# Kernel tuning notes

Hardware: AMD Instinct MI355X
Metric: run time of the kernel (lower is better)

Reference implementation:

```python
import jax, jax.numpy as jnp
import numpy as np

VOCAB, EMBED, HIDDEN = 32000, 512, 1024
BATCH, SRC_LEN = 64, 1024

def _xavier(key, shape):
    fan_out, fan_in = shape
    bound = float(np.sqrt(6.0 / (fan_in + fan_out)))
    return jax.random.uniform(key, shape, jnp.float32, -bound, bound)

def setup_inputs() -> dict:
    key = jax.random.key(0)
    k0, k1, k2, k3, k4 = jax.random.split(key, 5)
    src = jax.random.randint(k0, (BATCH, SRC_LEN), 0, VOCAB)
    emb = jax.random.normal(k1, (VOCAB, EMBED), jnp.float32)  # nn.Embedding default N(0,1)
    Wx = _xavier(k2, (4 * HIDDEN, EMBED))                     # x2h weight (out,in)
    bx = jax.random.uniform(k3, (4 * HIDDEN,), jnp.float32,
                            -1.0 / np.sqrt(EMBED), 1.0 / np.sqrt(EMBED))  # Linear default bias init
    Wh = _xavier(k4, (4 * HIDDEN, HIDDEN))                    # h2h weight, no bias
    return {"src": src, "emb": emb, "Wx": Wx, "bx": bx, "Wh": Wh}

def reference(src, emb, Wx, bx, Wh):
    B, T = src.shape
    H = Wh.shape[1]
    embedded = emb[src]                      # (B, T, E)
    # Precompute input projections for all steps: (T, B, 4H)
    x_proj = jnp.einsum('bte,ge->tbg', embedded, Wx) + bx

    def step(carry, xg):
        h, c = carry
        gates = xg + h @ Wh.T                # (B, 4H)
        i, f, o, g = jnp.split(gates, 4, axis=1)
        i = jax.nn.sigmoid(i)
        f = jax.nn.sigmoid(f)
        o = jax.nn.sigmoid(o)
        g = jnp.tanh(g)
        c = f * c + i * g
        h = o * jnp.tanh(c)
        return (h, c), None

    init = (jnp.zeros((B, H), jnp.float32), jnp.zeros((B, H), jnp.float32))
    (h_t, c_t), _ = jax.lax.scan(step, init, x_proj)
    return (h_t, c_t)
```

## Files before the change

### kernel.cpp

```cpp
#include <hip/hip_runtime.h>

typedef unsigned short u16;
typedef unsigned int   u32;
typedef unsigned long long u64;
typedef __attribute__((ext_vector_type(8))) __bf16 bf16x8;
typedef __attribute__((ext_vector_type(4))) float   f32x4;

#define B_   64
#define H_   1024
#define E_   512
#define G4_  4096
#define T_   1024
#define NWG  64

__device__ __forceinline__ u16 f2b(float f){
  union { float f; u32 u; } v; v.f = f;
  u32 r = v.u + 0x7fffu + ((v.u >> 16) & 1u);
  return (u16)(r >> 16);
}
__device__ __forceinline__ float b2f(u16 u){
  union { u32 u; float f; } v; v.u = ((u32)u) << 16;
  return v.f;
}
__device__ __forceinline__ float sigf(float x){
  return 1.0f / (1.0f + __expf(-x));
}
__device__ __forceinline__ float tanhf_s(float x){
  float ax = fabsf(x);
  float e  = __expf(2.0f * ax);
  float t  = 1.0f - 2.0f / (e + 1.0f);
  return copysignf(t, x);
}
__device__ __forceinline__ void gload_lds16(const void* g, void* l){
  __builtin_amdgcn_global_load_lds(
      (const __attribute__((address_space(1))) u32*)g,
      (__attribute__((address_space(3))) u32*)l, 16, 0, 0);
}

__global__ __launch_bounds__(256) void cvt_bf16(const float* __restrict__ in,
                                                u16* __restrict__ out, int n){
  int i = (blockIdx.x * 256 + threadIdx.x) * 4;
  if (i >= n) return;
  float4 v = *reinterpret_cast<const float4*>(in + i);
  ushort4 o;
  o.x = f2b(v.x); o.y = f2b(v.y); o.z = f2b(v.z); o.w = f2b(v.w);
  *reinterpret_cast<ushort4*>(out + i) = o;
}

__global__ __launch_bounds__(256) void emb_gather(const int* __restrict__ src,
                                                  const float* __restrict__ emb,
                                                  u16* __restrict__ embSeg, int t0){
  int idx = blockIdx.x * 256 + threadIdx.x;
  int m  = idx >> 7;
  int e4 = (idx & 127) << 2;
  int b = m & 63, ts = m >> 6;
  int tok = src[b * T_ + t0 + ts];
  float4 v = *reinterpret_cast<const float4*>(emb + (size_t)tok * E_ + e4);
  ushort4 o;
  o.x = f2b(v.x); o.y = f2b(v.y); o.z = f2b(v.z); o.w = f2b(v.w);
  *reinterpret_cast<ushort4*>(embSeg + (size_t)m * E_ + e4) = o;
}

__global__ __launch_bounds__(256) void xproj_gemm(const u16* __restrict__ embSeg,
                                                  const u16* __restrict__ WxB,
                                                  const float* __restrict__ bx,
                                                  u16* __restrict__ xp){
  __shared__ alignas(16) u16 Al[2][128][64];
  __shared__ alignas(16) u16 Bl[2][128][64];
  const int tid  = threadIdx.x;
  const int lane = tid & 63, wv = tid >> 6;
  const int wm = wv >> 1, wn = wv & 1;
  const int m0 = blockIdx.y * 128, n0 = blockIdx.x * 128;

  const int srow_w = wv * 8 + (lane >> 3);
  const int csrc   = (lane & 7) ^ (lane >> 3);

  auto stage = [&](int buf, int kb){
    const int kbase = kb * 64 + csrc * 8;
    #pragma unroll
    for (int it = 0; it < 4; ++it){
      const u16* ga = embSeg + (size_t)(m0 + it * 32 + srow_w) * E_ + kbase;
      gload_lds16(ga, &Al[buf][it * 32 + wv * 8][0]);
    }
    #pragma unroll
    for (int it = 0; it < 4; ++it){
      const u16* gb = WxB + (size_t)(n0 + it * 32 + srow_w) * E_ + kbase;
      gload_lds16(gb, &Bl[buf][it * 32 + wv * 8][0]);
    }
  };

  f32x4 acc[4][4] = {};
  stage(0, 0);
  __syncthreads();
  for (int kb = 0; kb < 8; ++kb){
    const int cur = kb & 1;
    if (kb < 7) stage(cur ^ 1, kb + 1);
    #pragma unroll
    for (int kk = 0; kk < 2; ++kk){
      bf16x8 af[4], bfr[4];
      #pragma unroll
      for (int i = 0; i < 4; ++i){
        int row = wm * 64 + i * 16 + (lane & 15);
        int cp  = (kk * 4 + (lane >> 4)) ^ (row & 7);
        af[i] = *reinterpret_cast<const bf16x8*>(&Al[cur][row][cp * 8]);
      }
      #pragma unroll
      for (int j = 0; j < 4; ++j){
        int row = wn * 64 + j * 16 + (lane & 15);
        int cp  = (kk * 4 + (lane >> 4)) ^ (row & 7);
        bfr[j] = *reinterpret_cast<const bf16x8*>(&Bl[cur][row][cp * 8]);
      }
      #pragma unroll
      for (int i = 0; i < 4; ++i)
        #pragma unroll
        for (int j = 0; j < 4; ++j)
          acc[i][j] = __builtin_amdgcn_mfma_f32_16x16x32_bf16(af[i], bfr[j], acc[i][j], 0, 0, 0);
    }
    __syncthreads();
  }

  float bxv[4];
  #pragma unroll
  for (int j = 0; j < 4; ++j) bxv[j] = bx[n0 + wn * 64 + j * 16 + (lane & 15)];
  #pragma unroll
  for (int i = 0; i < 4; ++i){
    int mrow = m0 + wm * 64 + i * 16 + ((lane >> 4) << 2);
    #pragma unroll
    for (int r = 0; r < 4; ++r){
      size_t base = (size_t)(mrow + r) * G4_ + n0 + wn * 64 + (lane & 15);
      #pragma unroll
      for (int j = 0; j < 4; ++j)
        xp[base + j * 16] = f2b(acc[i][j][r] + bxv[j]);
    }
  }
}

__global__ __launch_bounds__(256, 1) void lstm_rec(const float* __restrict__ Wh,
                                                   const u16* __restrict__ xp,
                                                   u16* __restrict__ hring,
                                                   float* __restrict__ c_state,
                                                   u32* __restrict__ cnt,
                                                   float* __restrict__ out,
                                                   int t0, int t1, int segm1){
  __shared__ alignas(16) u16 Wl[64][1024];
  const int tid  = threadIdx.x;
  const int lane = tid & 63, wv = tid >> 6;
  const int wg   = blockIdx.x;

  for (int it = tid; it < 64 * 128; it += 256){
    int r = it >> 7, c = it & 127;
    int gc = c ^ (r & 7);
    const float* gsrc = Wh + ((size_t)(r >> 4) * H_ + wg * 16 + (r & 15)) * H_ + gc * 8;
    float4 a = *reinterpret_cast<const float4*>(gsrc);
    float4 d = *reinterpret_cast<const float4*>(gsrc + 4);
    union { u16 s[8]; uint4 q; } u;
    u.s[0]=f2b(a.x); u.s[1]=f2b(a.y); u.s[2]=f2b(a.z); u.s[3]=f2b(a.w);
    u.s[4]=f2b(d.x); u.s[5]=f2b(d.y); u.s[6]=f2b(d.z); u.s[7]=f2b(d.w);
    *reinterpret_cast<uint4*>(&Wl[r][c * 8]) = u.q;
  }
  __syncthreads();

  const int b     = wv * 16 + (lane & 15);
  const int jbase = (lane >> 4) << 2;

  float cst[4];
  if (t0 == 0){
    cst[0] = cst[1] = cst[2] = cst[3] = 0.f;
  } else {
    float4 cv = *reinterpret_cast<const float4*>(c_state + (size_t)b * H_ + wg * 16 + jbase);
    cst[0] = cv.x; cst[1] = cv.y; cst[2] = cv.z; cst[3] = cv.w;
  }

  for (int t = t0; t < t1; ++t){
    const int ts = t - t0;
    ushort4 xv[4];
    const u16* xrow = xp + ((size_t)ts * B_ + b) * G4_ + wg * 16 + jbase;
    #pragma unroll
    for (int q = 0; q < 4; ++q)
      xv[q] = *reinterpret_cast<const ushort4*>(xrow + q * H_);

    f32x4 acc[4] = {};
    if (t > 0){
      const u32* cp = cnt + (t - 1);
      while (__hip_atomic_load(cp, __ATOMIC_RELAXED, __HIP_MEMORY_SCOPE_AGENT) < (u32)NWG) { }
      asm volatile("" ::: "memory");

      const u16* hp = hring + (size_t)((t - 1) & segm1) * (B_ * H_)
                    + (size_t)b * H_ + ((lane >> 4) << 3);
      uint4 hq[32];
      #pragma unroll
      for (int ks = 0; ks < 32; ++ks)
        hq[ks] = *reinterpret_cast<const uint4*>(hp + ks * 32);

      #pragma unroll
      for (int ks = 0; ks < 32; ++ks){
        union { uint4 q; bf16x8 v; } u; u.q = hq[ks];
        #pragma unroll
        for (int m = 0; m < 4; ++m){
          int row = m * 16 + (lane & 15);
          int cp2 = (ks * 4 + (lane >> 4)) ^ (row & 7);
          bf16x8 aw = *reinterpret_cast<const bf16x8*>(&Wl[row][cp2 * 8]);
          acc[m] = __builtin_amdgcn_mfma_f32_16x16x32_bf16(aw, u.v, acc[m], 0, 0, 0);
        }
      }
    }

    float hv[4];
    #pragma unroll
    for (int r = 0; r < 4; ++r){
      u16 x0 = (r==0)?xv[0].x:(r==1)?xv[0].y:(r==2)?xv[0].z:xv[0].w;
      u16 x1 = (r==0)?xv[1].x:(r==1)?xv[1].y:(r==2)?xv[1].z:xv[1].w;
      u16 x2 = (r==0)?xv[2].x:(r==1)?xv[2].y:(r==2)?xv[2].z:xv[2].w;
      u16 x3 = (r==0)?xv[3].x:(r==1)?xv[3].y:(r==2)?xv[3].z:xv[3].w;
      float gi = sigf(acc[0][r] + b2f(x0));
      float gf = sigf(acc[1][r] + b2f(x1));
      float go = sigf(acc[2][r] + b2f(x2));
      float gg = tanhf_s(acc[3][r] + b2f(x3));
      cst[r] = (t == 0) ? gi * gg : gf * cst[r] + gi * gg;
      hv[r]  = go * tanhf_s(cst[r]);
    }

    if (t < T_ - 1){
      u64 pk =  (u64)f2b(hv[0])
             | ((u64)f2b(hv[1]) << 16)
             | ((u64)f2b(hv[2]) << 32)
             | ((u64)f2b(hv[3]) << 48);
      u64* hd = (u64*)(hring + (size_t)(t & segm1) * (B_ * H_)
                       + (size_t)b * H_ + wg * 16 + jbase);
      __hip_atomic_store(hd, pk, __ATOMIC_RELAXED, __HIP_MEMORY_SCOPE_AGENT);
      asm volatile("s_waitcnt vmcnt(0)" ::: "memory");
      __syncthreads();
      if (tid == 0)
        __hip_atomic_fetch_add(cnt + t, 1u, __ATOMIC_RELAXED, __HIP_MEMORY_SCOPE_AGENT);
    } else {
      float4 ho; ho.x = hv[0]; ho.y = hv[1]; ho.z = hv[2]; ho.w = hv[3];
      float4 co; co.x = cst[0]; co.y = cst[1]; co.z = cst[2]; co.w = cst[3];
      *reinterpret_cast<float4*>(out + (size_t)b * H_ + wg * 16 + jbase) = ho;
      *reinterpret_cast<float4*>(out + (size_t)(B_ * H_) + (size_t)b * H_ + wg * 16 + jbase) = co;
    }
  }

  if (t1 < T_){
    float4 cv; cv.x = cst[0]; cv.y = cst[1]; cv.z = cst[2]; cv.w = cst[3];
    *reinterpret_cast<float4*>(c_state + (size_t)b * H_ + wg * 16 + jbase) = cv;
  }
}

extern "C" void kernel_launch(void* const* d_in, const int* in_sizes, int n_in,
                              void* d_out, int out_size, void* d_ws, size_t ws_size,
                              hipStream_t stream){
  const int*   src = (const int*)  d_in[0];
  const float* emb = (const float*)d_in[1];
  const float* Wx  = (const float*)d_in[2];
  const float* bx  = (const float*)d_in[3];
  const float* Wh  = (const float*)d_in[4];

  const size_t FIXED = 4194304 + 262144 + 4096;
  const size_t PERSEG = 65536 + 524288 + 131072;
  int SEG = 64;
  if (ws_size < FIXED + 64 * PERSEG){
    if      (ws_size >= FIXED + 16 * PERSEG) SEG = 16;
    else if (ws_size >= FIXED + 4  * PERSEG) SEG = 4;
    else                                     SEG = 2;
  }

  char*  ws      = (char*)d_ws;
  u16*   WxB     = (u16*)(ws);
  u16*   embSeg  = (u16*)(ws + 4194304);
  u16*   xpSeg   = (u16*)(ws + 4194304 + (size_t)SEG * 65536);
  u16*   hring   = (u16*)(ws + 4194304 + (size_t)SEG * 589824);
  float* c_state = (float*)(ws + 4194304 + (size_t)SEG * 720896);
  u32*   cnt     = (u32*) (ws + 4194304 + (size_t)SEG * 720896 + 262144);

  hipMemsetAsync(cnt, 0, T_ * 4, stream);
  cvt_bf16<<<2048, 256, 0, stream>>>(Wx, WxB, G4_ * E_);

  const int nseg = T_ / SEG;
  for (int s = 0; s < nseg; ++s){
    const int t0   = s * SEG;
    const int rows = SEG * B_;
    emb_gather<<<rows / 2, 256, 0, stream>>>(src, emb, embSeg, t0);
    dim3 g(G4_ / 128, rows / 128);
    xproj_gemm<<<g, 256, 0, stream>>>(embSeg, WxB, bx, xpSeg);
    lstm_rec<<<NWG, 256, 0, stream>>>(Wh, xpSeg, hring, c_state, cnt,
                                      (float*)d_out, t0, t0 + SEG, SEG - 1);
  }
}
```

Measured before the change: 7.454 ms.

## Replace per-step atomic counter barrier with per-wave flags and split MFMA chains

The per-step grid barrier changes from a single counter that every workgroup atomically increments to an array of per-wave flags. Each wave stores its own flag without a block-wide __syncthreads, and readers poll all 256 flags together with a wave-wide vote. The LDS swizzle widens from 8 to 16 columns to cut bank conflicts, and the MFMA accumulation is split into two independent chains to shorten the dependency. In exchange the flag array costs 1 MB of workspace and needs a larger memset, and each poll reads more memory.

```diff
diff --git a/kernel.cpp b/kernel.cpp
--- a/kernel.cpp
+++ b/kernel.cpp
@@ -139,7 +139,7 @@
                                                    const u16* __restrict__ xp,
                                                    u16* __restrict__ hring,
                                                    float* __restrict__ c_state,
-                                                   u32* __restrict__ cnt,
+                                                   u32* __restrict__ flags,
                                                    float* __restrict__ out,
                                                    int t0, int t1, int segm1){
   __shared__ alignas(16) u16 Wl[64][1024];
@@ -149,7 +149,7 @@
 
   for (int it = tid; it < 64 * 128; it += 256){
     int r = it >> 7, c = it & 127;
-    int gc = c ^ (r & 7);
+    int gc = c ^ (r & 15);
     const float* gsrc = Wh + ((size_t)(r >> 4) * H_ + wg * 16 + (r & 15)) * H_ + gc * 8;
     float4 a = *reinterpret_cast<const float4*>(gsrc);
     float4 d = *reinterpret_cast<const float4*>(gsrc + 4);
@@ -162,6 +162,7 @@
 
   const int b     = wv * 16 + (lane & 15);
   const int jbase = (lane >> 4) << 2;
+  const u64 ONE2  = 0x0000000100000001ULL;
 
   float cst[4];
   if (t0 == 0){
@@ -181,8 +182,12 @@
 
     f32x4 acc[4] = {};
     if (t > 0){
-      const u32* cp = cnt + (t - 1);
-      while (__hip_atomic_load(cp, __ATOMIC_RELAXED, __HIP_MEMORY_SCOPE_AGENT) < (u32)NWG) { }
+      const u64* fl = (const u64*)(flags + (size_t)(t - 1) * 256) + lane * 2;
+      for (;;){
+        u64 a  = __hip_atomic_load(fl,     __ATOMIC_RELAXED, __HIP_MEMORY_SCOPE_AGENT);
+        u64 b2 = __hip_atomic_load(fl + 1, __ATOMIC_RELAXED, __HIP_MEMORY_SCOPE_AGENT);
+        if (__all(a == ONE2 && b2 == ONE2)) break;
+      }
       asm volatile("" ::: "memory");
 
       const u16* hp = hring + (size_t)((t - 1) & segm1) * (B_ * H_)
@@ -192,17 +197,31 @@
       for (int ks = 0; ks < 32; ++ks)
         hq[ks] = *reinterpret_cast<const uint4*>(hp + ks * 32);
 
-      #pragma unroll
-      for (int ks = 0; ks < 32; ++ks){
+      f32x4 accA[4] = {}, accB[4] = {};
+      #pragma unroll
+      for (int ks = 0; ks < 16; ++ks){
         union { uint4 q; bf16x8 v; } u; u.q = hq[ks];
         #pragma unroll
         for (int m = 0; m < 4; ++m){
           int row = m * 16 + (lane & 15);
-          int cp2 = (ks * 4 + (lane >> 4)) ^ (row & 7);
+          int cp2 = (ks * 4 + (lane >> 4)) ^ (row & 15);
           bf16x8 aw = *reinterpret_cast<const bf16x8*>(&Wl[row][cp2 * 8]);
-          acc[m] = __builtin_amdgcn_mfma_f32_16x16x32_bf16(aw, u.v, acc[m], 0, 0, 0);
+          accA[m] = __builtin_amdgcn_mfma_f32_16x16x32_bf16(aw, u.v, accA[m], 0, 0, 0);
         }
       }
+      #pragma unroll
+      for (int ks = 16; ks < 32; ++ks){
+        union { uint4 q; bf16x8 v; } u; u.q = hq[ks];
+        #pragma unroll
+        for (int m = 0; m < 4; ++m){
+          int row = m * 16 + (lane & 15);
+          int cp2 = (ks * 4 + (lane >> 4)) ^ (row & 15);
+          bf16x8 aw = *reinterpret_cast<const bf16x8*>(&Wl[row][cp2 * 8]);
+          accB[m] = __builtin_amdgcn_mfma_f32_16x16x32_bf16(aw, u.v, accB[m], 0, 0, 0);
+        }
+      }
+      #pragma unroll
+      for (int m = 0; m < 4; ++m) acc[m] = accA[m] + accB[m];
     }
 
     float hv[4];
@@ -229,9 +248,9 @@
                        + (size_t)b * H_ + wg * 16 + jbase);
       __hip_atomic_store(hd, pk, __ATOMIC_RELAXED, __HIP_MEMORY_SCOPE_AGENT);
       asm volatile("s_waitcnt vmcnt(0)" ::: "memory");
-      __syncthreads();
-      if (tid == 0)
-        __hip_atomic_fetch_add(cnt + t, 1u, __ATOMIC_RELAXED, __HIP_MEMORY_SCOPE_AGENT);
+      if (lane == 0)
+        __hip_atomic_store(flags + (size_t)t * 256 + wg * 4 + wv, 1u,
+                           __ATOMIC_RELAXED, __HIP_MEMORY_SCOPE_AGENT);
     } else {
       float4 ho; ho.x = hv[0]; ho.y = hv[1]; ho.z = hv[2]; ho.w = hv[3];
       float4 co; co.x = cst[0]; co.y = cst[1]; co.z = cst[2]; co.w = cst[3];
@@ -255,7 +274,7 @@
   const float* bx  = (const float*)d_in[3];
   const float* Wh  = (const float*)d_in[4];
 
-  const size_t FIXED = 4194304 + 262144 + 4096;
+  const size_t FIXED  = 4194304 + 262144 + 1048576;
   const size_t PERSEG = 65536 + 524288 + 131072;
   int SEG = 64;
   if (ws_size < FIXED + 64 * PERSEG){
@@ -270,9 +289,9 @@
   u16*   xpSeg   = (u16*)(ws + 4194304 + (size_t)SEG * 65536);
   u16*   hring   = (u16*)(ws + 4194304 + (size_t)SEG * 589824);
   float* c_state = (float*)(ws + 4194304 + (size_t)SEG * 720896);
-  u32*   cnt     = (u32*) (ws + 4194304 + (size_t)SEG * 720896 + 262144);
-
-  hipMemsetAsync(cnt, 0, T_ * 4, stream);
+  u32*   flags   = (u32*) (ws + 4194304 + (size_t)SEG * 720896 + 262144);
+
+  hipMemsetAsync(flags, 0, (size_t)T_ * 256 * 4, stream);
   cvt_bf16<<<2048, 256, 0, stream>>>(Wx, WxB, G4_ * E_);
 
   const int nseg = T_ / SEG;
@@ -282,7 +301,7 @@
     emb_gather<<<rows / 2, 256, 0, stream>>>(src, emb, embSeg, t0);
     dim3 g(G4_ / 128, rows / 128);
     xproj_gemm<<<g, 256, 0, stream>>>(embSeg, WxB, bx, xpSeg);
-    lstm_rec<<<NWG, 256, 0, stream>>>(Wh, xpSeg, hring, c_state, cnt,
+    lstm_rec<<<NWG, 256, 0, stream>>>(Wh, xpSeg, hring, c_state, flags,
                                       (float*)d_out, t0, t0 + SEG, SEG - 1);
   }
 }
```

Result: slower. 10.27 ms (+37.7%).
